# Optimization experiments

Measured on AMD Instinct MI355X. Metric: run time of the kernel, lower is better.

The kernel has to match this reference:

```python
import jax, jax.numpy as jnp
import numpy as np

B = 2048; SQ = 64; PC = 24; F = 16; H = 128; D = 256; T = 128; A = 4672
NSQ = B * SQ; NPC = B * PC


def setup_inputs() -> dict:
    key = jax.random.key(0)
    ks = iter(jax.random.split(key, 48))
    def nrm(shape, s=0.05):
        return jax.random.normal(next(ks), shape, dtype=jnp.float32) * s
    def edges(e_per, src_per, dst_per):
        # per-graph local edges: graph_offset + local node index
        g = jnp.repeat(jnp.arange(B), e_per)
        src = g * src_per + jax.random.randint(next(ks), (B * e_per,), 0, src_per)
        dst = g * dst_per + jax.random.randint(next(ks), (B * e_per,), 0, dst_per)
        return jnp.stack([src, dst]).astype(jnp.int32)
    gp = jnp.repeat(jnp.arange(B), PC)
    occ_src = jnp.arange(NPC, dtype=jnp.int32)                       # each piece occupies one square
    occ_dst = (gp * SQ + jax.random.randint(next(ks), (NPC,), 0, SQ)).astype(jnp.int32)
    ei_occ = jnp.stack([occ_src, occ_dst])                           # piece -> square
    ei_rev = ei_occ[::-1]                                            # square -> piece (rev_occupied_by)
    return dict(
        x_sq=jax.random.normal(next(ks), (NSQ, F), dtype=jnp.float32),
        x_pc=jax.random.normal(next(ks), (NPC, F), dtype=jnp.float32),
        W_in_sq=nrm((F, H)), b_in_sq=jnp.zeros((H,), jnp.float32),
        W_in_pc=nrm((F, H)), b_in_pc=jnp.zeros((H,), jnp.float32),
        W_adj=nrm((H, H)), W_occ=nrm((H, H)), W_att=nrm((H, H)), W_def=nrm((H, H)), W_rev=nrm((H, H)),
        W_out=nrm((H, D)), b_out=jnp.zeros((D,), jnp.float32),
        W_pt=nrm((D, T)), b_pt=jnp.zeros((T,), jnp.float32),
        W_vt=nrm((D, T)), b_vt=jnp.zeros((T,), jnp.float32),
        W_ph=nrm((T, A)), b_ph=jnp.zeros((A,), jnp.float32),
        W_vh=nrm((T, 1)), b_vh=jnp.zeros((1,), jnp.float32),
        ei_adj=edges(420, SQ, SQ),
        ei_occ=ei_occ,
        ei_att=edges(40, PC, PC),
        ei_def=edges(40, PC, PC),
        ei_rev=ei_rev,
        square_batch=jnp.repeat(jnp.arange(B), SQ).astype(jnp.int32),
        piece_batch=gp.astype(jnp.int32),
    )


def reference(x_sq, x_pc, W_in_sq, b_in_sq, W_in_pc, b_in_pc,
              W_adj, W_occ, W_att, W_def, W_rev, W_out, b_out,
              W_pt, b_pt, W_vt, b_vt, W_ph, b_ph, W_vh, b_vh,
              ei_adj, ei_occ, ei_att, ei_def, ei_rev, square_batch, piece_batch):
    gelu = jax.nn.gelu
    seg = jax.ops.segment_sum
    # per-node-type input encoders
    h_sq = gelu(x_sq @ W_in_sq + b_in_sq)          # [NSQ, H]
    h_pc = gelu(x_pc @ W_in_pc + b_in_pc)          # [NPC, H]
    # heterogeneous message passing: gather -> linear -> scatter-sum per edge type
    agg_sq = seg(h_sq[ei_adj[0]] @ W_adj, ei_adj[1], NSQ)
    agg_sq = agg_sq + seg(h_pc[ei_occ[0]] @ W_occ, ei_occ[1], NSQ)
    agg_pc = seg(h_pc[ei_att[0]] @ W_att, ei_att[1], NPC)
    agg_pc = agg_pc + seg(h_pc[ei_def[0]] @ W_def, ei_def[1], NPC)
    agg_pc = agg_pc + seg(h_sq[ei_rev[0]] @ W_rev, ei_rev[1], NPC)
    h_sq2 = gelu(h_sq + agg_sq)
    h_pc2 = gelu(h_pc + agg_pc)
    # project to embed_dim and mean-pool per graph
    out_sq = gelu(h_sq2 @ W_out + b_out)           # [NSQ, D]
    out_pc = gelu(h_pc2 @ W_out + b_out)           # [NPC, D]
    shared = seg(out_sq, square_batch, B) / SQ + seg(out_pc, piece_batch, B) / PC  # [B, D]
    # dual trunks + heads (exactly as in ChessNetwork.forward)
    policy_logits = gelu(shared @ W_pt + b_pt) @ W_ph + b_ph        # [B, 4672]
    value = jnp.tanh(gelu(shared @ W_vt + b_vt) @ W_vh + b_vh)      # [B, 1]
    return policy_logits, value
```

## Files before the change

### kernel.cpp

```cpp
#include <hip/hip_runtime.h>

#define BATCH 2048
#define SQN 64
#define PCN 24
#define FEAT 16
#define HID 128
#define DOUT 256
#define TDIM 128
#define ADIM 4672
#define NSQT (BATCH*SQN)
#define NPCT (BATCH*PCN)
#define E_ADJ 420
#define E_ATT 40
#define E_ADJ_TOT (BATCH*E_ADJ)
#define E_ATT_TOT (BATCH*E_ATT)

typedef unsigned short u16;
typedef unsigned int u32;
typedef __attribute__((ext_vector_type(8))) short bf16x8;
typedef __attribute__((ext_vector_type(8))) unsigned short u16x8;
typedef __attribute__((ext_vector_type(4))) float f32x4;
typedef __attribute__((ext_vector_type(2))) unsigned int u32x2;
typedef __attribute__((ext_vector_type(4))) unsigned int u32x4;

#define OFF_WADJ_H 0
#define OFF_WADJ_L 16384
#define OFF_WOCC_H 32768
#define OFF_WOCC_L 49152
#define OFF_WATT_H 65536
#define OFF_WATT_L 81920
#define OFF_WDEF_H 98304
#define OFF_WDEF_L 114688
#define OFF_WREV_H 131072
#define OFF_WREV_L 147456
#define OFF_WOUT_H 163840
#define OFF_WOUT_L 196608
#define OFF_WPH_H  229376
#define OFF_WPH_L  827392
#define OFF_WINSQ_H 1425408
#define OFF_WINSQ_L 1429504
#define OFF_WINPC_H 1433600
#define OFF_WINPC_L 1437696
#define WB_TOTAL    1441792

#define K_SMEM 81920

#define PHP_OFF  0
#define PAH_OFF  24576
#define PAL_OFF  36864
#define PEA_OFF  49152
#define PED_OFF  49472
#define PSA_OFF  49792
#define PSD_OFF  50112
#define PRSA_OFF 50432
#define PCUA_OFF 50692
#define PCNA_OFF 50948
#define PRSD_OFF 51204
#define PCUD_OFF 51464
#define PCND_OFF 51720
#define PRVS_OFF 51976
#define PRVD_OFF 52168

__device__ __forceinline__ u32 cvtpk(float a, float b) {
    u32 r;
    asm("v_cvt_pk_bf16_f32 %0, %1, %2" : "=v"(r) : "v"(a), "v"(b));
    return r;
}
__device__ __forceinline__ u16 f2b(float x) { return (u16)cvtpk(x, x); }
__device__ __forceinline__ float b2f(u16 h) { return __uint_as_float(((u32)h) << 16); }
__device__ __forceinline__ void split2(float x, u16& h, u16& l) {
    u32 wp = cvtpk(x, x);
    h = (u16)wp;
    float r = x - __uint_as_float(wp << 16);
    l = (u16)cvtpk(r, r);
}
__device__ __forceinline__ void split_pk(float a, float b, u32& wh, u32& wl) {
    wh = cvtpk(a, b);
    float ra = a - __uint_as_float(wh << 16);
    float rb = b - __uint_as_float(wh & 0xffff0000u);
    wl = cvtpk(ra, rb);
}
__device__ __forceinline__ float gelu_f(float x) {
    float x2 = x * x;
    float z2 = x * __builtin_fmaf(x2, 0.0713548162f, 1.5957691216f);
    float e = __expf(z2);
    return x - x * __fdividef(1.0f, e + 1.0f);
}
__device__ __forceinline__ f32x4 MFMA(bf16x8 a, bf16x8 b, f32x4 c) {
    return __builtin_amdgcn_mfma_f32_16x16x32_bf16(a, b, c, 0, 0, 0);
}
__device__ __forceinline__ bf16x8 bzero() {
    bf16x8 v = {0,0,0,0,0,0,0,0}; return v;
}
__device__ __forceinline__ void xfrag(const float* __restrict__ xrow, int g,
                                      bf16x8& ah, bf16x8& al)
{
    const f32x4 a = *(const f32x4*)(xrow + g*8);
    const f32x4 b = *(const f32x4*)(xrow + g*8 + 4);
    u32 h0,h1,h2,h3,l0,l1,l2,l3;
    split_pk(a[0], a[1], h0, l0);
    split_pk(a[2], a[3], h1, l1);
    split_pk(b[0], b[1], h2, l2);
    split_pk(b[2], b[3], h3, l3);
    u32x4 vh = {h0,h1,h2,h3};
    u32x4 vl = {l0,l1,l2,l3};
    ah = *(bf16x8*)&vh;
    al = *(bf16x8*)&vl;
}

template<int NT, int RT>
__device__ __forceinline__ void gemm_nt(
    const unsigned char* Ah, const unsigned char* Al,
    const u16* __restrict__ wh, const u16* __restrict__ wl,
    int ntBase, int lane, int g, int lr, f32x4 (&c)[NT][RT])
{
    const int sw = lr << 4;
    #pragma unroll
    for (int ks = 0; ks < 4; ++ks) {
        const int ko = ks*64 + g*16;
        bf16x8 ah[RT], al[RT];
        #pragma unroll
        for (int rt = 0; rt < RT; ++rt) {
            const int ro = (rt*16 + lr)*256 + (ko ^ sw);
            ah[rt] = *(const bf16x8*)(Ah + ro);
            al[rt] = *(const bf16x8*)(Al + ro);
        }
        #pragma unroll
        for (int ntl = 0; ntl < NT; ++ntl) {
            bf16x8 bh = *(const bf16x8*)(wh + (((ntBase+ntl)*4 + ks)*64 + lane)*8);
            bf16x8 bl = *(const bf16x8*)(wl + (((ntBase+ntl)*4 + ks)*64 + lane)*8);
            #pragma unroll
            for (int rt = 0; rt < RT; ++rt) {
                c[ntl][rt] = MFMA(ah[rt], bh, c[ntl][rt]);
                c[ntl][rt] = MFMA(al[rt], bh, c[ntl][rt]);
                c[ntl][rt] = MFMA(ah[rt], bl, c[ntl][rt]);
            }
        }
    }
}

__device__ __forceinline__ void gather_f32_8(
    const unsigned char* H, const int* srt, int st, int en, int cq8, float (&acc)[16])
{
    for (int i = st; i < en; ++i) {
        const int s = srt[i];
        const unsigned char* rp = H + s*512;
        const int sw2 = (s & 15) << 4;
        #pragma unroll
        for (int u = 0; u < 4; ++u) {
            f32x4 v = *(const f32x4*)(rp + ((cq8*64 + u*16) ^ sw2));
            acc[u*4+0] += v[0]; acc[u*4+1] += v[1];
            acc[u*4+2] += v[2]; acc[u*4+3] += v[3];
        }
    }
}
__device__ __forceinline__ void writeA_8(
    unsigned char* Ah, unsigned char* Al, int d, int cq8, const float (&acc)[16])
{
    unsigned char* wh = Ah + d*256;
    unsigned char* wl = Al + d*256;
    const int dw = (d & 15) << 4;
    #pragma unroll
    for (int u = 0; u < 2; ++u) {
        u32 oh[4], ol[4];
        #pragma unroll
        for (int j = 0; j < 4; ++j)
            split_pk(acc[u*8 + j*2], acc[u*8 + j*2 + 1], oh[j], ol[j]);
        u32x4 vh = {oh[0], oh[1], oh[2], oh[3]};
        u32x4 vl = {ol[0], ol[1], ol[2], ol[3]};
        *(u32x4*)(wh + ((cq8*32 + u*16) ^ dw)) = vh;
        *(u32x4*)(wl + ((cq8*32 + u*16) ^ dw)) = vl;
    }
}

__global__ __launch_bounds__(256) void k_prep(
    const float* __restrict__ W_adj, const float* __restrict__ W_occ,
    const float* __restrict__ W_att, const float* __restrict__ W_def,
    const float* __restrict__ W_rev, const float* __restrict__ W_out,
    const float* __restrict__ W_ph,
    const float* __restrict__ W_in_sq, const float* __restrict__ W_in_pc,
    u16* __restrict__ wb)
{
    int gid = blockIdx.x*256 + threadIdx.x;
    int fid = gid >> 6, lane = gid & 63;
    int g8 = (lane >> 4) * 8, lr = lane & 15;
    u16x8 vh, vl;
    if (fid >= 1392) {
        int f = fid - 1392;
        const float* src = (f < 8) ? W_in_sq : W_in_pc;
        int oh = (f < 8) ? OFF_WINSQ_H : OFF_WINPC_H;
        int ol = (f < 8) ? OFF_WINSQ_L : OFF_WINPC_L;
        int nt = f & 7;
        int col = nt*16 + lr;
        #pragma unroll
        for (int j = 0; j < 8; ++j) {
            int k = g8 + j;
            float v = (k < 16) ? src[k*HID + col] : 0.f;
            u16 h, l; split2(v, h, l);
            vh[j] = h; vl[j] = l;
        }
        *(u16x8*)(wb + oh + (nt*64 + lane)*8) = vh;
        *(u16x8*)(wb + ol + (nt*64 + lane)*8) = vl;
        return;
    }
    const float* src; int ld, f, oh, ol;
    if (fid < 32)       { src = W_adj; ld = HID;  f = fid;      oh = OFF_WADJ_H; ol = OFF_WADJ_L; }
    else if (fid < 64)  { src = W_occ; ld = HID;  f = fid-32;   oh = OFF_WOCC_H; ol = OFF_WOCC_L; }
    else if (fid < 96)  { src = W_att; ld = HID;  f = fid-64;   oh = OFF_WATT_H; ol = OFF_WATT_L; }
    else if (fid < 128) { src = W_def; ld = HID;  f = fid-96;   oh = OFF_WDEF_H; ol = OFF_WDEF_L; }
    else if (fid < 160) { src = W_rev; ld = HID;  f = fid-128;  oh = OFF_WREV_H; ol = OFF_WREV_L; }
    else if (fid < 224) { src = W_out; ld = DOUT; f = fid-160;  oh = OFF_WOUT_H; ol = OFF_WOUT_L; }
    else                { src = W_ph;  ld = ADIM; f = fid-224;  oh = OFF_WPH_H;  ol = OFF_WPH_L; }
    int nt = f >> 2, kb = f & 3;
    int col = nt*16 + lr;
    #pragma unroll
    for (int j = 0; j < 8; ++j) {
        int k = kb*32 + g8 + j;
        u16 h, l; split2(src[k*ld + col], h, l);
        vh[j] = h; vl[j] = l;
    }
    *(u16x8*)(wb + oh + (f*64 + lane)*8) = vh;
    *(u16x8*)(wb + ol + (f*64 + lane)*8) = vl;
}

__device__ __forceinline__ void sq_path(
    unsigned char* SMb, int b, int t,
    const float* __restrict__ x_sq, const float* __restrict__ x_pc,
    const float* __restrict__ b_in_sq, const float* __restrict__ b_in_pc,
    const float* __restrict__ b_out,
    const int* __restrict__ ei_adj, const int* __restrict__ ei_occ,
    const u16* __restrict__ wb, float* __restrict__ shared_sq)
{
    unsigned char* Hs_h  = SMb;
    unsigned char* Hs_l  = SMb + 16384;
    int*           Mint  = (int*)(SMb + 32768);
    unsigned char* HOT_h = SMb + 32768;
    unsigned char* HOT_l = SMb + 40960;
    unsigned char* Mocc  = SMb + 49152;
    unsigned char* A_h   = SMb + 32768;
    unsigned char* A_l   = SMb + 49152;
    unsigned char* Madj  = SMb + 65536;
    unsigned char* Hp    = SMb + 73728;

    const int w = t >> 6, lane = t & 63, g = lane >> 4, lr = lane & 15;
    const int colp = w*16 + lr;

    #pragma unroll
    for (int i = 0; i < 8; ++i) Mint[t + i*512] = 0;
    ((u32*)Mocc)[t] = 0;
    ((u32*)Mocc)[t + 512] = 0;
    ((u32*)(Hp + 6144))[t] = 0;
    __syncthreads();

    for (int i = t; i < E_ADJ; i += 512) {
        int s = ei_adj[b*E_ADJ + i] - b*SQN;
        int d = ei_adj[E_ADJ_TOT + b*E_ADJ + i] - b*SQN;
        atomicAdd(&Mint[d*64 + s], 1);
    }
    if (t < PCN) {
        int p = ei_occ[b*PCN + t] - b*PCN;
        int d = ei_occ[NPCT + b*PCN + t] - b*SQN;
        *(u16*)(Mocc + d*64 + ((p*2) ^ ((d&3)<<4))) = 0x3F80;
    }
    __syncthreads();

    #pragma unroll
    for (int ii = 0; ii < 4; ++ii) {
        int i = t + ii*512;
        int row = i >> 5, cp = i & 31;
        float v0 = (float)Mint[row*64 + cp*2];
        float v1 = (float)Mint[row*64 + cp*2 + 1];
        *(u32*)(Madj + row*128 + ((cp*4) ^ ((row&7)<<4))) = cvtpk(v0, v1);
    }
    float hv[16];
    {
        const f32x4 z = {0.f,0.f,0.f,0.f};
        f32x4 ch[4] = {z,z,z,z};
        {
            bf16x8 bh = *(const bf16x8*)(wb + OFF_WINSQ_H + (w*64 + lane)*8);
            bf16x8 bl = *(const bf16x8*)(wb + OFF_WINSQ_L + (w*64 + lane)*8);
            #pragma unroll
            for (int rt = 0; rt < 4; ++rt) {
                bf16x8 ah = bzero(), al = bzero();
                if (g < 2) xfrag(x_sq + (b*SQN + rt*16 + lr)*FEAT, g, ah, al);
                ch[rt] = MFMA(ah, bh, ch[rt]);
                ch[rt] = MFMA(al, bh, ch[rt]);
                ch[rt] = MFMA(ah, bl, ch[rt]);
            }
        }
        const float bbs = b_in_sq[colp];
        #pragma unroll
        for (int rt = 0; rt < 4; ++rt)
            #pragma unroll
            for (int r = 0; r < 4; ++r) {
                const int row = rt*16 + g*4 + r;
                float h = gelu_f(ch[rt][r] + bbs);
                hv[rt*4 + r] = h;
                u16 hh, ll; split2(h, hh, ll);
                const int bo = row*256 + ((colp*2) ^ ((row&15)<<4));
                *(u16*)(Hs_h + bo) = hh;
                *(u16*)(Hs_l + bo) = ll;
            }
        f32x4 cp2[2] = {z, z};
        {
            bf16x8 bh = *(const bf16x8*)(wb + OFF_WINPC_H + (w*64 + lane)*8);
            bf16x8 bl = *(const bf16x8*)(wb + OFF_WINPC_L + (w*64 + lane)*8);
            #pragma unroll
            for (int rt = 0; rt < 2; ++rt) {
                const int row = rt*16 + lr;
                bf16x8 ah = bzero(), al = bzero();
                if (g < 2 && row < PCN) xfrag(x_pc + (b*PCN + row)*FEAT, g, ah, al);
                cp2[rt] = MFMA(ah, bh, cp2[rt]);
                cp2[rt] = MFMA(al, bh, cp2[rt]);
                cp2[rt] = MFMA(ah, bl, cp2[rt]);
            }
        }
        const float bbp = b_in_pc[colp];
        #pragma unroll
        for (int rt = 0; rt < 2; ++rt)
            #pragma unroll
            for (int r = 0; r < 4; ++r) {
                const int row = rt*16 + g*4 + r;
                if (row < PCN) {
                    float h = gelu_f(cp2[rt][r] + bbp);
                    *(u16*)(Hp + row*256 + ((colp*2) ^ ((row&15)<<4))) = f2b(h);
                }
            }
    }
    __syncthreads();

    f32x4 hwj[4], hwo[2];
    {
        const f32x4 z = {0.f,0.f,0.f,0.f};
        hwj[0]=z; hwj[1]=z; hwj[2]=z; hwj[3]=z; hwo[0]=z; hwo[1]=z;
        const int sw15 = lr << 4;
        #pragma unroll
        for (int ks = 0; ks < 4; ++ks) {
            const int ko = ks*64 + g*16;
            bf16x8 bh = *(const bf16x8*)(wb + OFF_WADJ_H + ((w*4 + ks)*64 + lane)*8);
            bf16x8 bl = *(const bf16x8*)(wb + OFF_WADJ_L + ((w*4 + ks)*64 + lane)*8);
            #pragma unroll
            for (int rt = 0; rt < 4; ++rt) {
                const int ro = (rt*16 + lr)*256 + (ko ^ sw15);
                bf16x8 ah = *(const bf16x8*)(Hs_h + ro);
                bf16x8 al = *(const bf16x8*)(Hs_l + ro);
                hwj[rt] = MFMA(ah, bh, hwj[rt]);
                hwj[rt] = MFMA(al, bh, hwj[rt]);
                hwj[rt] = MFMA(ah, bl, hwj[rt]);
            }
            bf16x8 oh = *(const bf16x8*)(wb + OFF_WOCC_H + ((w*4 + ks)*64 + lane)*8);
            bf16x8 ol = *(const bf16x8*)(wb + OFF_WOCC_L + ((w*4 + ks)*64 + lane)*8);
            #pragma unroll
            for (int rt = 0; rt < 2; ++rt) {
                const int ro = (rt*16 + lr)*256 + (ko ^ sw15);
                bf16x8 ah = *(const bf16x8*)(Hp + ro);
                hwo[rt] = MFMA(ah, oh, hwo[rt]);
                hwo[rt] = MFMA(ah, ol, hwo[rt]);
            }
        }
    }
    __syncthreads();

    {
        const int swj = (lr & 7) << 4;
        #pragma unroll
        for (int rt = 0; rt < 4; ++rt) {
            u32 h01, l01, h23, l23;
            split_pk(hwj[rt][0], hwj[rt][1], h01, l01);
            split_pk(hwj[rt][2], hwj[rt][3], h23, l23);
            const int off = colp*128 + ((rt*32 + g*8) ^ swj);
            *(u32x2*)(Hs_h + off) = (u32x2){h01, h23};
            *(u32x2*)(Hs_l + off) = (u32x2){l01, l23};
        }
        const int swo = (lr & 3) << 4;
        #pragma unroll
        for (int rt = 0; rt < 2; ++rt) {
            u32 h01, l01, h23, l23;
            split_pk(hwo[rt][0], hwo[rt][1], h01, l01);
            split_pk(hwo[rt][2], hwo[rt][3], h23, l23);
            const int off = colp*64 + ((rt*32 + g*8) ^ swo);
            *(u32x2*)(HOT_h + off) = (u32x2){h01, h23};
            *(u32x2*)(HOT_l + off) = (u32x2){l01, l23};
        }
    }
    __syncthreads();

    f32x4 c1[4];
    {
        const f32x4 z = {0.f,0.f,0.f,0.f};
        c1[0]=z; c1[1]=z; c1[2]=z; c1[3]=z;
        const int swj = (lr & 7) << 4;
        #pragma unroll
        for (int ks = 0; ks < 2; ++ks) {
            const int bo = colp*128 + ((ks*64 + g*16) ^ swj);
            bf16x8 bh = *(const bf16x8*)(Hs_h + bo);
            bf16x8 bl = *(const bf16x8*)(Hs_l + bo);
            #pragma unroll
            for (int rt = 0; rt < 4; ++rt) {
                const int ao = (rt*16 + lr)*128 + ((ks*64 + g*16) ^ swj);
                bf16x8 am = *(const bf16x8*)(Madj + ao);
                c1[rt] = MFMA(am, bh, c1[rt]);
                c1[rt] = MFMA(am, bl, c1[rt]);
            }
        }
        const int swo = (lr & 3) << 4;
        {
            const int bo = colp*64 + ((g*16) ^ swo);
            bf16x8 bh = *(const bf16x8*)(HOT_h + bo);
            bf16x8 bl = *(const bf16x8*)(HOT_l + bo);
            #pragma unroll
            for (int rt = 0; rt < 4; ++rt) {
                const int ao = (rt*16 + lr)*64 + ((g*16) ^ swo);
                bf16x8 am = *(const bf16x8*)(Mocc + ao);
                c1[rt] = MFMA(am, bh, c1[rt]);
                c1[rt] = MFMA(am, bl, c1[rt]);
            }
        }
    }
    __syncthreads();

    #pragma unroll
    for (int rt = 0; rt < 4; ++rt)
        #pragma unroll
        for (int r = 0; r < 4; ++r) {
            const int row = rt*16 + g*4 + r;
            float h2 = gelu_f(c1[rt][r] + hv[rt*4 + r]);
            u16 hh, ll; split2(h2, hh, ll);
            const int bo = row*256 + ((colp*2) ^ ((row&15)<<4));
            *(u16*)(A_h + bo) = hh;
            *(u16*)(A_l + bo) = ll;
        }
    __syncthreads();

    f32x4 c2[2][4];
    {
        const f32x4 z = {0.f,0.f,0.f,0.f};
        #pragma unroll
        for (int n = 0; n < 2; ++n)
            #pragma unroll
            for (int rt = 0; rt < 4; ++rt) c2[n][rt] = z;
    }
    gemm_nt<2,4>(A_h, A_l, wb + OFF_WOUT_H, wb + OFF_WOUT_L, w*2, lane, g, lr, c2);
    #pragma unroll
    for (int ntl = 0; ntl < 2; ++ntl) {
        const int col = (w*2 + ntl)*16 + lr;
        const float bias = b_out[col];
        float cs = 0.f;
        #pragma unroll
        for (int rt = 0; rt < 4; ++rt)
            #pragma unroll
            for (int r = 0; r < 4; ++r) cs += gelu_f(c2[ntl][rt][r] + bias);
        cs += __shfl_xor(cs, 16);
        cs += __shfl_xor(cs, 32);
        if (lane < 16) shared_sq[b*DOUT + col] = cs * (1.0f/64.0f);
    }
}

__device__ __forceinline__ void pc_path(
    unsigned char* SMb, int pcb, int t,
    const float* __restrict__ x_sq, const float* __restrict__ x_pc,
    const float* __restrict__ b_in_sq, const float* __restrict__ b_in_pc,
    const float* __restrict__ b_out,
    const int* __restrict__ ei_att, const int* __restrict__ ei_def,
    const int* __restrict__ ei_rev,
    const u16* __restrict__ wb, float* __restrict__ shared_pc)
{
    unsigned char* Hp = SMb + PHP_OFF;
    unsigned char* Ah = SMb + PAH_OFF;
    unsigned char* Al = SMb + PAL_OFF;
    int* ea_pk = (int*)(SMb + PEA_OFF);
    int* ed_pk = (int*)(SMb + PED_OFF);
    int* srt_a = (int*)(SMb + PSA_OFF);
    int* srt_d = (int*)(SMb + PSD_OFF);
    int* rs_a  = (int*)(SMb + PRSA_OFF);
    int* cur_a = (int*)(SMb + PCUA_OFF);
    int* cnt_a = (int*)(SMb + PCNA_OFF);
    int* rs_d  = (int*)(SMb + PRSD_OFF);
    int* cur_d = (int*)(SMb + PCUD_OFF);
    int* cnt_d = (int*)(SMb + PCND_OFF);
    int* rv_s  = (int*)(SMb + PRVS_OFF);
    int* rv_d  = (int*)(SMb + PRVD_OFF);

    const int w = t >> 6, lane = t & 63, g = lane >> 4, lr = lane & 15;
    const int NR = 2*PCN;

    for (int i = t; i < 2*E_ATT; i += 512) {
        int sb = (i >= E_ATT) ? 1 : 0;
        int e = i - sb*E_ATT;
        int gb = pcb*2 + sb;
        int ro = sb*PCN - gb*PCN;
        int s = ei_att[gb*E_ATT + e] + ro;
        int d = ei_att[E_ATT_TOT + gb*E_ATT + e] + ro;
        ea_pk[i] = s | (d << 16);
        s = ei_def[gb*E_ATT + e] + ro;
        d = ei_def[E_ATT_TOT + gb*E_ATT + e] + ro;
        ed_pk[i] = s | (d << 16);
    }
    if (t < NR) {
        int sb = (t >= PCN) ? 1 : 0;
        int gb = pcb*2 + sb;
        int p = t - sb*PCN;
        rv_s[t] = ei_rev[gb*PCN + p];
        rv_d[t] = ei_rev[NPCT + gb*PCN + p] - gb*PCN + sb*PCN;
    }
    if (t < 64) { cnt_a[t] = 0; cnt_d[t] = 0; }
    __syncthreads();

    for (int i = t; i < 2*E_ATT; i += 512) {
        atomicAdd(&cnt_a[ea_pk[i] >> 16], 1);
        atomicAdd(&cnt_d[ed_pk[i] >> 16], 1);
    }
    __syncthreads();

    if (t < 64) {
        int v = cnt_a[t], o0 = v;
        for (int o = 1; o < 64; o <<= 1) { int u = __shfl_up(v, o); if (t >= o) v += u; }
        rs_a[t+1] = v; cur_a[t] = v - o0; if (t == 0) rs_a[0] = 0;
    } else if (t < 128) {
        int l = t - 64;
        int v = cnt_d[l], o0 = v;
        for (int o = 1; o < 64; o <<= 1) { int u = __shfl_up(v, o); if (l >= o) v += u; }
        rs_d[l+1] = v; cur_d[l] = v - o0; if (l == 0) rs_d[0] = 0;
    }
    __syncthreads();

    for (int i = t; i < 2*E_ATT; i += 512) {
        int pk = ea_pk[i];
        int p = atomicAdd(&cur_a[pk >> 16], 1); srt_a[p] = pk & 0xffff;
        pk = ed_pk[i];
        p = atomicAdd(&cur_d[pk >> 16], 1); srt_d[p] = pk & 0xffff;
    }
    {
        const int colp = w*16 + lr;
        const f32x4 z = {0.f,0.f,0.f,0.f};
        f32x4 cp[3] = {z,z,z};
        {
            bf16x8 bh = *(const bf16x8*)(wb + OFF_WINPC_H + (w*64 + lane)*8);
            bf16x8 bl = *(const bf16x8*)(wb + OFF_WINPC_L + (w*64 + lane)*8);
            #pragma unroll
            for (int rt = 0; rt < 3; ++rt) {
                bf16x8 ah = bzero(), al = bzero();
                if (g < 2) xfrag(x_pc + (pcb*NR + rt*16 + lr)*FEAT, g, ah, al);
                cp[rt] = MFMA(ah, bh, cp[rt]);
                cp[rt] = MFMA(al, bh, cp[rt]);
                cp[rt] = MFMA(ah, bl, cp[rt]);
            }
        }
        const float bbp = b_in_pc[colp];
        #pragma unroll
        for (int rt = 0; rt < 3; ++rt)
            #pragma unroll
            for (int r = 0; r < 4; ++r) {
                const int row = rt*16 + g*4 + r;
                float h = gelu_f(cp[rt][r] + bbp);
                *(float*)(Hp + row*512 + ((colp*4) ^ ((row&15)<<4))) = h;
            }
        f32x4 cr[3] = {z,z,z};
        {
            bf16x8 bh = *(const bf16x8*)(wb + OFF_WINSQ_H + (w*64 + lane)*8);
            bf16x8 bl = *(const bf16x8*)(wb + OFF_WINSQ_L + (w*64 + lane)*8);
            #pragma unroll
            for (int rt = 0; rt < 3; ++rt) {
                bf16x8 ah = bzero(), al = bzero();
                if (g < 2) {
                    int gr = rv_s[rt*16 + lr];
                    xfrag(x_sq + gr*FEAT, g, ah, al);
                }
                cr[rt] = MFMA(ah, bh, cr[rt]);
                cr[rt] = MFMA(al, bh, cr[rt]);
                cr[rt] = MFMA(ah, bl, cr[rt]);
            }
        }
        const float bbs = b_in_sq[colp];
        #pragma unroll
        for (int rt = 0; rt < 3; ++rt)
            #pragma unroll
            for (int r = 0; r < 4; ++r) {
                const int row0 = rt*16 + g*4 + r;
                const int dr = rv_d[row0];
                float h = gelu_f(cr[rt][r] + bbs);
                u16 hh, ll; split2(h, hh, ll);
                const int bo = dr*256 + ((colp*2) ^ ((dr&15)<<4));
                *(u16*)(Ah + bo) = hh;
                *(u16*)(Al + bo) = ll;
            }
    }
    __syncthreads();

    f32x4 c1[1][3];
    {
        const f32x4 z = {0.f,0.f,0.f,0.f};
        #pragma unroll
        for (int rt = 0; rt < 3; ++rt) c1[0][rt] = z;
    }
    gemm_nt<1,3>(Ah, Al, wb + OFF_WREV_H, wb + OFF_WREV_L, w, lane, g, lr, c1);
    __syncthreads();

    {
        const int d = t >> 3, cq8 = t & 7;
        if (d < NR) {
            float acc[16];
            #pragma unroll
            for (int i = 0; i < 16; ++i) acc[i] = 0.f;
            gather_f32_8(Hp, srt_a, rs_a[d], rs_a[d+1], cq8, acc);
            writeA_8(Ah, Al, d, cq8, acc);
        }
    }
    __syncthreads();

    gemm_nt<1,3>(Ah, Al, wb + OFF_WATT_H, wb + OFF_WATT_L, w, lane, g, lr, c1);
    __syncthreads();

    {
        const int d = t >> 3, cq8 = t & 7;
        if (d < NR) {
            float acc[16];
            #pragma unroll
            for (int i = 0; i < 16; ++i) acc[i] = 0.f;
            gather_f32_8(Hp, srt_d, rs_d[d], rs_d[d+1], cq8, acc);
            writeA_8(Ah, Al, d, cq8, acc);
        }
    }
    __syncthreads();

    gemm_nt<1,3>(Ah, Al, wb + OFF_WDEF_H, wb + OFF_WDEF_L, w, lane, g, lr, c1);
    __syncthreads();

    {
        const int colp = w*16 + lr;
        #pragma unroll
        for (int rt = 0; rt < 3; ++rt)
            #pragma unroll
            for (int r = 0; r < 4; ++r) {
                const int row = rt*16 + g*4 + r;
                float hvv = *(const float*)(Hp + row*512 + ((colp*4) ^ ((row&15)<<4)));
                float h2 = gelu_f(c1[0][rt][r] + hvv);
                u16 hh, ll; split2(h2, hh, ll);
                const int bo = row*256 + ((colp*2) ^ ((row&15)<<4));
                *(u16*)(Ah + bo) = hh;
                *(u16*)(Al + bo) = ll;
            }
    }
    __syncthreads();

    f32x4 c2[2][3];
    {
        const f32x4 z = {0.f,0.f,0.f,0.f};
        #pragma unroll
        for (int n = 0; n < 2; ++n)
            #pragma unroll
            for (int rt = 0; rt < 3; ++rt) c2[n][rt] = z;
    }
    gemm_nt<2,3>(Ah, Al, wb + OFF_WOUT_H, wb + OFF_WOUT_L, w*2, lane, g, lr, c2);
    #pragma unroll
    for (int ntl = 0; ntl < 2; ++ntl) {
        const int col = (w*2 + ntl)*16 + lr;
        const float bias = b_out[col];
        float s0 = 0.f, s1 = 0.f;
        #pragma unroll
        for (int r = 0; r < 4; ++r) s0 += gelu_f(c2[ntl][0][r] + bias);
        {
            float tt = 0.f;
            #pragma unroll
            for (int r = 0; r < 4; ++r) tt += gelu_f(c2[ntl][1][r] + bias);
            s0 += (g < 2) ? tt : 0.f;
            s1 += (g < 2) ? 0.f : tt;
        }
        #pragma unroll
        for (int r = 0; r < 4; ++r) s1 += gelu_f(c2[ntl][2][r] + bias);
        s0 += __shfl_xor(s0, 16); s0 += __shfl_xor(s0, 32);
        s1 += __shfl_xor(s1, 16); s1 += __shfl_xor(s1, 32);
        if (lane < 16) {
            const int b0 = pcb*2, b1 = b0 + 1;
            shared_pc[b0*DOUT + col] = s0 * (1.0f/PCN);
            shared_pc[b1*DOUT + col] = s1 * (1.0f/PCN);
        }
    }
}

__global__ __launch_bounds__(512, 4) void k_main(
    const float* __restrict__ x_sq, const float* __restrict__ x_pc,
    const float* __restrict__ b_in_sq, const float* __restrict__ b_in_pc,
    const float* __restrict__ b_out,
    const int* __restrict__ ei_adj, const int* __restrict__ ei_occ,
    const int* __restrict__ ei_att, const int* __restrict__ ei_def,
    const int* __restrict__ ei_rev,
    const u16* __restrict__ wb,
    float* __restrict__ shared_sq, float* __restrict__ shared_pc)
{
    extern __shared__ __align__(16) unsigned char SMb[];
    const int bid = blockIdx.x;
    const int grp = bid / 3, rem = bid - grp*3;
    if (rem < 2) {
        sq_path(SMb, grp*2 + rem, threadIdx.x, x_sq, x_pc, b_in_sq, b_in_pc,
                b_out, ei_adj, ei_occ, wb, shared_sq);
    } else {
        pc_path(SMb, grp, threadIdx.x, x_sq, x_pc, b_in_sq, b_in_pc,
                b_out, ei_att, ei_def, ei_rev, wb, shared_pc);
    }
}

__global__ __launch_bounds__(256) void k_head(
    const float* __restrict__ shared_sq, const float* __restrict__ shared_pc,
    const float* __restrict__ W_pt, const float* __restrict__ b_pt,
    const float* __restrict__ W_vt, const float* __restrict__ b_vt,
    const float* __restrict__ W_vh, const float* __restrict__ b_vh,
    u16* __restrict__ tpol_h, u16* __restrict__ tpol_l, float* __restrict__ out_value)
{
    __shared__ float sh[2*DOUT];
    __shared__ float vred[2*TDIM];
    const int t = threadIdx.x;
    const int hh = t >> 7, j = t & 127;
    const int b = blockIdx.x*2 + hh;
    for (int i = t; i < 2*DOUT; i += 256)
        sh[i] = shared_sq[blockIdx.x*2*DOUT + i] + shared_pc[blockIdx.x*2*DOUT + i];
    __syncthreads();
    const float* s = sh + hh*DOUT;
    float ap = b_pt[j], av = b_vt[j];
    #pragma unroll 8
    for (int k = 0; k < DOUT; ++k) {
        float sv = s[k];
        ap += sv * W_pt[k*TDIM + j];
        av += sv * W_vt[k*TDIM + j];
    }
    float tv = gelu_f(ap);
    u16 th, tl; split2(tv, th, tl);
    tpol_h[b*TDIM + j] = th;
    tpol_l[b*TDIM + j] = tl;
    vred[hh*TDIM + j] = gelu_f(av) * W_vh[j];
    __syncthreads();
    for (int stp = 64; stp > 0; stp >>= 1) {
        if (j < stp) vred[hh*TDIM + j] += vred[hh*TDIM + j + stp];
        __syncthreads();
    }
    if (j == 0) out_value[b] = tanhf(vred[hh*TDIM] + b_vh[0]);
}

__global__ __launch_bounds__(256) void k_pol(
    const u16* __restrict__ tpol_h, const u16* __restrict__ tpol_l,
    const u16* __restrict__ wb, const float* __restrict__ b_ph,
    float* __restrict__ pol)
{
    const u16* wph_h = wb + OFF_WPH_H;
    const u16* wph_l = wb + OFF_WPH_L;
    const int t = threadIdx.x, w = t >> 6, lane = t & 63, g = lane >> 4, lr = lane & 15;
    const int nt = blockIdx.x*4 + w;
    const int rbase = blockIdx.y*64;
    f32x4 acc[4];
    const f32x4 z = {0.f,0.f,0.f,0.f};
    #pragma unroll
    for (int rt = 0; rt < 4; ++rt) acc[rt] = z;
    #pragma unroll
    for (int ks = 0; ks < 4; ++ks) {
        bf16x8 bh = *(const bf16x8*)(wph_h + ((nt*4 + ks)*64 + lane)*8);
        bf16x8 bl = *(const bf16x8*)(wph_l + ((nt*4 + ks)*64 + lane)*8);
        #pragma unroll
        for (int rt = 0; rt < 4; ++rt) {
            const int ro = (rbase + rt*16 + lr)*TDIM + ks*32 + g*8;
            bf16x8 ah = *(const bf16x8*)(tpol_h + ro);
            bf16x8 al = *(const bf16x8*)(tpol_l + ro);
            acc[rt] = MFMA(ah, bh, acc[rt]);
            acc[rt] = MFMA(al, bh, acc[rt]);
            acc[rt] = MFMA(ah, bl, acc[rt]);
        }
    }
    const float bias = b_ph[nt*16 + lr];
    #pragma unroll
    for (int rt = 0; rt < 4; ++rt)
        #pragma unroll
        for (int r = 0; r < 4; ++r) {
            int row = rbase + rt*16 + g*4 + r;
            pol[(size_t)row*ADIM + nt*16 + lr] = acc[rt][r] + bias;
        }
}

extern "C" void kernel_launch(void* const* d_in, const int* in_sizes, int n_in,
                              void* d_out, int out_size, void* d_ws, size_t ws_size,
                              hipStream_t stream) {
    (void)in_sizes; (void)n_in; (void)out_size; (void)ws_size;
    const float* x_sq    = (const float*)d_in[0];
    const float* x_pc    = (const float*)d_in[1];
    const float* W_in_sq = (const float*)d_in[2];
    const float* b_in_sq = (const float*)d_in[3];
    const float* W_in_pc = (const float*)d_in[4];
    const float* b_in_pc = (const float*)d_in[5];
    const float* W_adj   = (const float*)d_in[6];
    const float* W_occ   = (const float*)d_in[7];
    const float* W_att   = (const float*)d_in[8];
    const float* W_def   = (const float*)d_in[9];
    const float* W_rev   = (const float*)d_in[10];
    const float* W_out   = (const float*)d_in[11];
    const float* b_out   = (const float*)d_in[12];
    const float* W_pt    = (const float*)d_in[13];
    const float* b_pt    = (const float*)d_in[14];
    const float* W_vt    = (const float*)d_in[15];
    const float* b_vt    = (const float*)d_in[16];
    const float* W_ph    = (const float*)d_in[17];
    const float* b_ph    = (const float*)d_in[18];
    const float* W_vh    = (const float*)d_in[19];
    const float* b_vh    = (const float*)d_in[20];
    const int* ei_adj    = (const int*)d_in[21];
    const int* ei_occ    = (const int*)d_in[22];
    const int* ei_att    = (const int*)d_in[23];
    const int* ei_def    = (const int*)d_in[24];
    const int* ei_rev    = (const int*)d_in[25];

    float* out = (float*)d_out;
    float* pol = out;
    float* val = out + (size_t)BATCH * ADIM;

    float* shared_sq = (float*)d_ws;
    float* shared_pc = shared_sq + BATCH*DOUT;
    u16* tpol_h = (u16*)(shared_pc + BATCH*DOUT);
    u16* tpol_l = tpol_h + BATCH*TDIM;
    u16* wb     = tpol_l + BATCH*TDIM;

    hipFuncSetAttribute((const void*)k_main,
                        hipFuncAttributeMaxDynamicSharedMemorySize, K_SMEM);

    k_prep<<<352, 256, 0, stream>>>(W_adj, W_occ, W_att, W_def, W_rev, W_out, W_ph,
                                    W_in_sq, W_in_pc, wb);
    k_main<<<3072, 512, K_SMEM, stream>>>(x_sq, x_pc, b_in_sq, b_in_pc, b_out,
                                          ei_adj, ei_occ, ei_att, ei_def, ei_rev,
                                          wb, shared_sq, shared_pc);
    k_head<<<BATCH/2, 256, 0, stream>>>(shared_sq, shared_pc, W_pt, b_pt, W_vt, b_vt,
                                        W_vh, b_vh, tpol_h, tpol_l, val);
    k_pol<<<dim3(ADIM/64, BATCH/64), 256, 0, stream>>>(tpol_h, tpol_l, wb, b_ph, pol);
}
```

Before: 198.2 us.

## Double k_main threads per block and move trunk GEMMs to MFMA

k_main now launches 1024 threads per block instead of 512. Wave work is re-split so each wave covers half the row tiles of one column tile, and the pc path's shared-memory layout is enlarged. Separately, the policy and value trunk projections in k_head become split-bf16 MFMA GEMMs over 32-row tiles, with weights pre-packed in k_prep, replacing the scalar per-thread dot products. The aim is more waves in flight per block and tensor-core use in the head, at the cost of more A-fragment reloads from LDS and possible occupancy limits at 1024 threads with 80KB LDS.

```diff
diff --git a/kernel.cpp b/kernel.cpp
--- a/kernel.cpp
+++ b/kernel.cpp
@@ -41,25 +41,29 @@
 #define OFF_WINSQ_L 1429504
 #define OFF_WINPC_H 1433600
 #define OFF_WINPC_L 1437696
-#define WB_TOTAL    1441792
+#define OFF_WPT_H  1441792
+#define OFF_WPT_L  1474560
+#define OFF_WVT_H  1507328
+#define OFF_WVT_L  1540096
+#define WB_TOTAL   1572864
 
 #define K_SMEM 81920
 
 #define PHP_OFF  0
-#define PAH_OFF  24576
-#define PAL_OFF  36864
-#define PEA_OFF  49152
-#define PED_OFF  49472
-#define PSA_OFF  49792
-#define PSD_OFF  50112
-#define PRSA_OFF 50432
-#define PCUA_OFF 50692
-#define PCNA_OFF 50948
-#define PRSD_OFF 51204
-#define PCUD_OFF 51464
-#define PCND_OFF 51720
-#define PRVS_OFF 51976
-#define PRVD_OFF 52168
+#define PAH_OFF  32768
+#define PAL_OFF  49152
+#define PEA_OFF  65536
+#define PED_OFF  65856
+#define PSA_OFF  66176
+#define PSD_OFF  66496
+#define PRSA_OFF 66816
+#define PCUA_OFF 67076
+#define PCNA_OFF 67332
+#define PRSD_OFF 67588
+#define PCUD_OFF 67848
+#define PCND_OFF 68104
+#define PRVS_OFF 68360
+#define PRVD_OFF 68616
 
 __device__ __forceinline__ u32 cvtpk(float a, float b) {
     u32 r;
@@ -112,65 +116,55 @@
 __device__ __forceinline__ void gemm_nt(
     const unsigned char* Ah, const unsigned char* Al,
     const u16* __restrict__ wh, const u16* __restrict__ wl,
-    int ntBase, int lane, int g, int lr, f32x4 (&c)[NT][RT])
+    int ntBase, int rowBase, int lane, int g, int lr, f32x4 (&c)[NT][RT])
 {
     const int sw = lr << 4;
     #pragma unroll
     for (int ks = 0; ks < 4; ++ks) {
-        const int ko = ks*64 + g*16;
-        bf16x8 ah[RT], al[RT];
-        #pragma unroll
-        for (int rt = 0; rt < RT; ++rt) {
-            const int ro = (rt*16 + lr)*256 + (ko ^ sw);
-            ah[rt] = *(const bf16x8*)(Ah + ro);
-            al[rt] = *(const bf16x8*)(Al + ro);
-        }
+        const int ko = (ks*64 + g*16) ^ sw;
         #pragma unroll
         for (int ntl = 0; ntl < NT; ++ntl) {
             bf16x8 bh = *(const bf16x8*)(wh + (((ntBase+ntl)*4 + ks)*64 + lane)*8);
             bf16x8 bl = *(const bf16x8*)(wl + (((ntBase+ntl)*4 + ks)*64 + lane)*8);
             #pragma unroll
             for (int rt = 0; rt < RT; ++rt) {
-                c[ntl][rt] = MFMA(ah[rt], bh, c[ntl][rt]);
-                c[ntl][rt] = MFMA(al[rt], bh, c[ntl][rt]);
-                c[ntl][rt] = MFMA(ah[rt], bl, c[ntl][rt]);
-            }
-        }
-    }
-}
-
-__device__ __forceinline__ void gather_f32_8(
-    const unsigned char* H, const int* srt, int st, int en, int cq8, float (&acc)[16])
+                const int ro = ((rowBase+rt)*16 + lr)*256 + ko;
+                bf16x8 ah = *(const bf16x8*)(Ah + ro);
+                bf16x8 al = *(const bf16x8*)(Al + ro);
+                c[ntl][rt] = MFMA(ah, bh, c[ntl][rt]);
+                c[ntl][rt] = MFMA(al, bh, c[ntl][rt]);
+                c[ntl][rt] = MFMA(ah, bl, c[ntl][rt]);
+            }
+        }
+    }
+}
+
+__device__ __forceinline__ void gather_f32_16(
+    const unsigned char* H, const int* srt, int st, int en, int cq, float (&acc)[8])
 {
     for (int i = st; i < en; ++i) {
         const int s = srt[i];
         const unsigned char* rp = H + s*512;
         const int sw2 = (s & 15) << 4;
         #pragma unroll
-        for (int u = 0; u < 4; ++u) {
-            f32x4 v = *(const f32x4*)(rp + ((cq8*64 + u*16) ^ sw2));
+        for (int u = 0; u < 2; ++u) {
+            f32x4 v = *(const f32x4*)(rp + ((cq*32 + u*16) ^ sw2));
             acc[u*4+0] += v[0]; acc[u*4+1] += v[1];
             acc[u*4+2] += v[2]; acc[u*4+3] += v[3];
         }
     }
 }
-__device__ __forceinline__ void writeA_8(
-    unsigned char* Ah, unsigned char* Al, int d, int cq8, const float (&acc)[16])
-{
-    unsigned char* wh = Ah + d*256;
-    unsigned char* wl = Al + d*256;
+__device__ __forceinline__ void writeA_16(
+    unsigned char* Ah, unsigned char* Al, int d, int cq, const float (&acc)[8])
+{
     const int dw = (d & 15) << 4;
-    #pragma unroll
-    for (int u = 0; u < 2; ++u) {
-        u32 oh[4], ol[4];
-        #pragma unroll
-        for (int j = 0; j < 4; ++j)
-            split_pk(acc[u*8 + j*2], acc[u*8 + j*2 + 1], oh[j], ol[j]);
-        u32x4 vh = {oh[0], oh[1], oh[2], oh[3]};
-        u32x4 vl = {ol[0], ol[1], ol[2], ol[3]};
-        *(u32x4*)(wh + ((cq8*32 + u*16) ^ dw)) = vh;
-        *(u32x4*)(wl + ((cq8*32 + u*16) ^ dw)) = vl;
-    }
+    u32 oh[4], ol[4];
+    #pragma unroll
+    for (int j = 0; j < 4; ++j) split_pk(acc[j*2], acc[j*2+1], oh[j], ol[j]);
+    u32x4 vh = {oh[0],oh[1],oh[2],oh[3]};
+    u32x4 vl = {ol[0],ol[1],ol[2],ol[3]};
+    *(u32x4*)(Ah + d*256 + ((cq*16) ^ dw)) = vh;
+    *(u32x4*)(Al + d*256 + ((cq*16) ^ dw)) = vl;
 }
 
 __global__ __launch_bounds__(256) void k_prep(
@@ -179,12 +173,31 @@
     const float* __restrict__ W_rev, const float* __restrict__ W_out,
     const float* __restrict__ W_ph,
     const float* __restrict__ W_in_sq, const float* __restrict__ W_in_pc,
+    const float* __restrict__ W_pt, const float* __restrict__ W_vt,
     u16* __restrict__ wb)
 {
     int gid = blockIdx.x*256 + threadIdx.x;
     int fid = gid >> 6, lane = gid & 63;
     int g8 = (lane >> 4) * 8, lr = lane & 15;
     u16x8 vh, vl;
+    if (fid >= 1408) {
+        int f = fid - 1408;
+        int which = f >> 6, f2 = f & 63;
+        const float* src = which ? W_vt : W_pt;
+        int oh = which ? OFF_WVT_H : OFF_WPT_H;
+        int ol = which ? OFF_WVT_L : OFF_WPT_L;
+        int nt = f2 >> 3, kb = f2 & 7;
+        int col = nt*16 + lr;
+        #pragma unroll
+        for (int j = 0; j < 8; ++j) {
+            int k = kb*32 + g8 + j;
+            u16 h, l; split2(src[k*TDIM + col], h, l);
+            vh[j] = h; vl[j] = l;
+        }
+        *(u16x8*)(wb + oh + (f2*64 + lane)*8) = vh;
+        *(u16x8*)(wb + ol + (f2*64 + lane)*8) = vl;
+        return;
+    }
     if (fid >= 1392) {
         int f = fid - 1392;
         const float* src = (f < 8) ? W_in_sq : W_in_pc;
@@ -243,16 +256,16 @@
     unsigned char* Hp    = SMb + 73728;
 
     const int w = t >> 6, lane = t & 63, g = lane >> 4, lr = lane & 15;
-    const int colp = w*16 + lr;
-
-    #pragma unroll
-    for (int i = 0; i < 8; ++i) Mint[t + i*512] = 0;
+    const int n2 = w >> 1, rh = w & 1, rtb = rh*2;
+    const int colp = n2*16 + lr;
+
+    #pragma unroll
+    for (int ii = 0; ii < 4; ++ii) Mint[t + ii*1024] = 0;
     ((u32*)Mocc)[t] = 0;
-    ((u32*)Mocc)[t + 512] = 0;
-    ((u32*)(Hp + 6144))[t] = 0;
-    __syncthreads();
-
-    for (int i = t; i < E_ADJ; i += 512) {
+    if (t < 512) ((u32*)(Hp + 6144))[t] = 0;
+    __syncthreads();
+
+    for (int i = t; i < E_ADJ; i += 1024) {
         int s = ei_adj[b*E_ADJ + i] - b*SQN;
         int d = ei_adj[E_ADJ_TOT + b*E_ADJ + i] - b*SQN;
         atomicAdd(&Mint[d*64 + s], 1);
@@ -265,24 +278,24 @@
     __syncthreads();
 
     #pragma unroll
-    for (int ii = 0; ii < 4; ++ii) {
-        int i = t + ii*512;
+    for (int ii = 0; ii < 2; ++ii) {
+        int i = t + ii*1024;
         int row = i >> 5, cp = i & 31;
         float v0 = (float)Mint[row*64 + cp*2];
         float v1 = (float)Mint[row*64 + cp*2 + 1];
         *(u32*)(Madj + row*128 + ((cp*4) ^ ((row&7)<<4))) = cvtpk(v0, v1);
     }
-    float hv[16];
+    float hv[8];
     {
         const f32x4 z = {0.f,0.f,0.f,0.f};
-        f32x4 ch[4] = {z,z,z,z};
+        f32x4 ch[2] = {z,z};
         {
-            bf16x8 bh = *(const bf16x8*)(wb + OFF_WINSQ_H + (w*64 + lane)*8);
-            bf16x8 bl = *(const bf16x8*)(wb + OFF_WINSQ_L + (w*64 + lane)*8);
-            #pragma unroll
-            for (int rt = 0; rt < 4; ++rt) {
+            bf16x8 bh = *(const bf16x8*)(wb + OFF_WINSQ_H + (n2*64 + lane)*8);
+            bf16x8 bl = *(const bf16x8*)(wb + OFF_WINSQ_L + (n2*64 + lane)*8);
+            #pragma unroll
+            for (int rt = 0; rt < 2; ++rt) {
                 bf16x8 ah = bzero(), al = bzero();
-                if (g < 2) xfrag(x_sq + (b*SQN + rt*16 + lr)*FEAT, g, ah, al);
+                if (g < 2) xfrag(x_sq + (b*SQN + (rtb+rt)*16 + lr)*FEAT, g, ah, al);
                 ch[rt] = MFMA(ah, bh, ch[rt]);
                 ch[rt] = MFMA(al, bh, ch[rt]);
                 ch[rt] = MFMA(ah, bl, ch[rt]);
@@ -290,10 +303,10 @@
         }
         const float bbs = b_in_sq[colp];
         #pragma unroll
-        for (int rt = 0; rt < 4; ++rt)
+        for (int rt = 0; rt < 2; ++rt)
             #pragma unroll
             for (int r = 0; r < 4; ++r) {
-                const int row = rt*16 + g*4 + r;
+                const int row = (rtb+rt)*16 + g*4 + r;
                 float h = gelu_f(ch[rt][r] + bbs);
                 hv[rt*4 + r] = h;
                 u16 hh, ll; split2(h, hh, ll);
@@ -301,61 +314,55 @@
                 *(u16*)(Hs_h + bo) = hh;
                 *(u16*)(Hs_l + bo) = ll;
             }
-        f32x4 cp2[2] = {z, z};
+        f32x4 cp2 = z;
         {
-            bf16x8 bh = *(const bf16x8*)(wb + OFF_WINPC_H + (w*64 + lane)*8);
-            bf16x8 bl = *(const bf16x8*)(wb + OFF_WINPC_L + (w*64 + lane)*8);
+            bf16x8 bh = *(const bf16x8*)(wb + OFF_WINPC_H + (n2*64 + lane)*8);
+            bf16x8 bl = *(const bf16x8*)(wb + OFF_WINPC_L + (n2*64 + lane)*8);
+            const int row0 = rh*16 + lr;
+            bf16x8 ah = bzero(), al = bzero();
+            if (g < 2 && row0 < PCN) xfrag(x_pc + (b*PCN + row0)*FEAT, g, ah, al);
+            cp2 = MFMA(ah, bh, cp2);
+            cp2 = MFMA(al, bh, cp2);
+            cp2 = MFMA(ah, bl, cp2);
+        }
+        const float bbp = b_in_pc[colp];
+        #pragma unroll
+        for (int r = 0; r < 4; ++r) {
+            const int row = rh*16 + g*4 + r;
+            if (row < PCN) {
+                float h = gelu_f(cp2[r] + bbp);
+                *(u16*)(Hp + row*256 + ((colp*2) ^ ((row&15)<<4))) = f2b(h);
+            }
+        }
+    }
+    __syncthreads();
+
+    f32x4 hwj[2], hwo;
+    {
+        const f32x4 z = {0.f,0.f,0.f,0.f};
+        hwj[0]=z; hwj[1]=z; hwo=z;
+        const int sw15 = lr << 4;
+        #pragma unroll
+        for (int ks = 0; ks < 4; ++ks) {
+            const int ko = (ks*64 + g*16) ^ sw15;
+            bf16x8 bh = *(const bf16x8*)(wb + OFF_WADJ_H + ((n2*4 + ks)*64 + lane)*8);
+            bf16x8 bl = *(const bf16x8*)(wb + OFF_WADJ_L + ((n2*4 + ks)*64 + lane)*8);
             #pragma unroll
             for (int rt = 0; rt < 2; ++rt) {
-                const int row = rt*16 + lr;
-                bf16x8 ah = bzero(), al = bzero();
-                if (g < 2 && row < PCN) xfrag(x_pc + (b*PCN + row)*FEAT, g, ah, al);
-                cp2[rt] = MFMA(ah, bh, cp2[rt]);
-                cp2[rt] = MFMA(al, bh, cp2[rt]);
-                cp2[rt] = MFMA(ah, bl, cp2[rt]);
-            }
-        }
-        const float bbp = b_in_pc[colp];
-        #pragma unroll
-        for (int rt = 0; rt < 2; ++rt)
-            #pragma unroll
-            for (int r = 0; r < 4; ++r) {
-                const int row = rt*16 + g*4 + r;
-                if (row < PCN) {
-                    float h = gelu_f(cp2[rt][r] + bbp);
-                    *(u16*)(Hp + row*256 + ((colp*2) ^ ((row&15)<<4))) = f2b(h);
-                }
-            }
-    }
-    __syncthreads();
-
-    f32x4 hwj[4], hwo[2];
-    {
-        const f32x4 z = {0.f,0.f,0.f,0.f};
-        hwj[0]=z; hwj[1]=z; hwj[2]=z; hwj[3]=z; hwo[0]=z; hwo[1]=z;
-        const int sw15 = lr << 4;
-        #pragma unroll
-        for (int ks = 0; ks < 4; ++ks) {
-            const int ko = ks*64 + g*16;
-            bf16x8 bh = *(const bf16x8*)(wb + OFF_WADJ_H + ((w*4 + ks)*64 + lane)*8);
-            bf16x8 bl = *(const bf16x8*)(wb + OFF_WADJ_L + ((w*4 + ks)*64 + lane)*8);
-            #pragma unroll
-            for (int rt = 0; rt < 4; ++rt) {
-                const int ro = (rt*16 + lr)*256 + (ko ^ sw15);
+                const int ro = ((rtb+rt)*16 + lr)*256 + ko;
                 bf16x8 ah = *(const bf16x8*)(Hs_h + ro);
                 bf16x8 al = *(const bf16x8*)(Hs_l + ro);
                 hwj[rt] = MFMA(ah, bh, hwj[rt]);
                 hwj[rt] = MFMA(al, bh, hwj[rt]);
                 hwj[rt] = MFMA(ah, bl, hwj[rt]);
             }
-            bf16x8 oh = *(const bf16x8*)(wb + OFF_WOCC_H + ((w*4 + ks)*64 + lane)*8);
-            bf16x8 ol = *(const bf16x8*)(wb + OFF_WOCC_L + ((w*4 + ks)*64 + lane)*8);
-            #pragma unroll
-            for (int rt = 0; rt < 2; ++rt) {
-                const int ro = (rt*16 + lr)*256 + (ko ^ sw15);
+            bf16x8 oh = *(const bf16x8*)(wb + OFF_WOCC_H + ((n2*4 + ks)*64 + lane)*8);
+            bf16x8 ol = *(const bf16x8*)(wb + OFF_WOCC_L + ((n2*4 + ks)*64 + lane)*8);
+            {
+                const int ro = (rh*16 + lr)*256 + ko;
                 bf16x8 ah = *(const bf16x8*)(Hp + ro);
-                hwo[rt] = MFMA(ah, oh, hwo[rt]);
-                hwo[rt] = MFMA(ah, ol, hwo[rt]);
+                hwo = MFMA(ah, oh, hwo);
+                hwo = MFMA(ah, ol, hwo);
             }
         }
     }
@@ -364,31 +371,30 @@
     {
         const int swj = (lr & 7) << 4;
         #pragma unroll
-        for (int rt = 0; rt < 4; ++rt) {
+        for (int rt = 0; rt < 2; ++rt) {
             u32 h01, l01, h23, l23;
             split_pk(hwj[rt][0], hwj[rt][1], h01, l01);
             split_pk(hwj[rt][2], hwj[rt][3], h23, l23);
-            const int off = colp*128 + ((rt*32 + g*8) ^ swj);
+            const int off = colp*128 + (((rtb+rt)*32 + g*8) ^ swj);
             *(u32x2*)(Hs_h + off) = (u32x2){h01, h23};
             *(u32x2*)(Hs_l + off) = (u32x2){l01, l23};
         }
         const int swo = (lr & 3) << 4;
-        #pragma unroll
-        for (int rt = 0; rt < 2; ++rt) {
+        {
             u32 h01, l01, h23, l23;
-            split_pk(hwo[rt][0], hwo[rt][1], h01, l01);
-            split_pk(hwo[rt][2], hwo[rt][3], h23, l23);
-            const int off = colp*64 + ((rt*32 + g*8) ^ swo);
+            split_pk(hwo[0], hwo[1], h01, l01);
+            split_pk(hwo[2], hwo[3], h23, l23);
+            const int off = colp*64 + ((rh*32 + g*8) ^ swo);
             *(u32x2*)(HOT_h + off) = (u32x2){h01, h23};
             *(u32x2*)(HOT_l + off) = (u32x2){l01, l23};
         }
     }
     __syncthreads();
 
-    f32x4 c1[4];
+    f32x4 c1[2];
     {
         const f32x4 z = {0.f,0.f,0.f,0.f};
-        c1[0]=z; c1[1]=z; c1[2]=z; c1[3]=z;
+        c1[0]=z; c1[1]=z;
         const int swj = (lr & 7) << 4;
         #pragma unroll
         for (int ks = 0; ks < 2; ++ks) {
@@ -396,8 +402,8 @@
             bf16x8 bh = *(const bf16x8*)(Hs_h + bo);
             bf16x8 bl = *(const bf16x8*)(Hs_l + bo);
             #pragma unroll
-            for (int rt = 0; rt < 4; ++rt) {
-                const int ao = (rt*16 + lr)*128 + ((ks*64 + g*16) ^ swj);
+            for (int rt = 0; rt < 2; ++rt) {
+                const int ao = ((rtb+rt)*16 + lr)*128 + ((ks*64 + g*16) ^ swj);
                 bf16x8 am = *(const bf16x8*)(Madj + ao);
                 c1[rt] = MFMA(am, bh, c1[rt]);
                 c1[rt] = MFMA(am, bl, c1[rt]);
@@ -409,8 +415,8 @@
             bf16x8 bh = *(const bf16x8*)(HOT_h + bo);
             bf16x8 bl = *(const bf16x8*)(HOT_l + bo);
             #pragma unroll
-            for (int rt = 0; rt < 4; ++rt) {
-                const int ao = (rt*16 + lr)*64 + ((g*16) ^ swo);
+            for (int rt = 0; rt < 2; ++rt) {
+                const int ao = ((rtb+rt)*16 + lr)*64 + ((g*16) ^ swo);
                 bf16x8 am = *(const bf16x8*)(Mocc + ao);
                 c1[rt] = MFMA(am, bh, c1[rt]);
                 c1[rt] = MFMA(am, bl, c1[rt]);
@@ -420,10 +426,10 @@
     __syncthreads();
 
     #pragma unroll
-    for (int rt = 0; rt < 4; ++rt)
+    for (int rt = 0; rt < 2; ++rt)
         #pragma unroll
         for (int r = 0; r < 4; ++r) {
-            const int row = rt*16 + g*4 + r;
+            const int row = (rtb+rt)*16 + g*4 + r;
             float h2 = gelu_f(c1[rt][r] + hv[rt*4 + r]);
             u16 hh, ll; split2(h2, hh, ll);
             const int bo = row*256 + ((colp*2) ^ ((row&15)<<4));
@@ -432,24 +438,21 @@
         }
     __syncthreads();
 
-    f32x4 c2[2][4];
+    f32x4 c2[1][4];
     {
         const f32x4 z = {0.f,0.f,0.f,0.f};
         #pragma unroll
-        for (int n = 0; n < 2; ++n)
-            #pragma unroll
-            for (int rt = 0; rt < 4; ++rt) c2[n][rt] = z;
-    }
-    gemm_nt<2,4>(A_h, A_l, wb + OFF_WOUT_H, wb + OFF_WOUT_L, w*2, lane, g, lr, c2);
-    #pragma unroll
-    for (int ntl = 0; ntl < 2; ++ntl) {
-        const int col = (w*2 + ntl)*16 + lr;
+        for (int rt = 0; rt < 4; ++rt) c2[0][rt] = z;
+    }
+    gemm_nt<1,4>(A_h, A_l, wb + OFF_WOUT_H, wb + OFF_WOUT_L, w, 0, lane, g, lr, c2);
+    {
+        const int col = w*16 + lr;
         const float bias = b_out[col];
         float cs = 0.f;
         #pragma unroll
         for (int rt = 0; rt < 4; ++rt)
             #pragma unroll
-            for (int r = 0; r < 4; ++r) cs += gelu_f(c2[ntl][rt][r] + bias);
+            for (int r = 0; r < 4; ++r) cs += gelu_f(c2[0][rt][r] + bias);
         cs += __shfl_xor(cs, 16);
         cs += __shfl_xor(cs, 32);
         if (lane < 16) shared_sq[b*DOUT + col] = cs * (1.0f/64.0f);
@@ -482,13 +485,14 @@
     int* rv_d  = (int*)(SMb + PRVD_OFF);
 
     const int w = t >> 6, lane = t & 63, g = lane >> 4, lr = lane & 15;
-    const int NR = 2*PCN;
-
-    for (int i = t; i < 2*E_ATT; i += 512) {
+    const int n2 = w >> 1, rh = w & 1, rtb = rh*2;
+    const int colp = n2*16 + lr;
+
+    for (int i = t; i < 2*E_ATT; i += 1024) {
         int sb = (i >= E_ATT) ? 1 : 0;
         int e = i - sb*E_ATT;
         int gb = pcb*2 + sb;
-        int ro = sb*PCN - gb*PCN;
+        int ro = 32*sb - gb*PCN;
         int s = ei_att[gb*E_ATT + e] + ro;
         int d = ei_att[E_ATT_TOT + gb*E_ATT + e] + ro;
         ea_pk[i] = s | (d << 16);
@@ -496,17 +500,17 @@
         d = ei_def[E_ATT_TOT + gb*E_ATT + e] + ro;
         ed_pk[i] = s | (d << 16);
     }
-    if (t < NR) {
-        int sb = (t >= PCN) ? 1 : 0;
-        int gb = pcb*2 + sb;
-        int p = t - sb*PCN;
-        rv_s[t] = ei_rev[gb*PCN + p];
-        rv_d[t] = ei_rev[NPCT + gb*PCN + p] - gb*PCN + sb*PCN;
-    }
-    if (t < 64) { cnt_a[t] = 0; cnt_d[t] = 0; }
-    __syncthreads();
-
-    for (int i = t; i < 2*E_ATT; i += 512) {
+    if (t < 64) {
+        int sb = t >> 5, pr = t & 31, gb = pcb*2 + sb;
+        if (pr < PCN) {
+            rv_s[t] = ei_rev[gb*PCN + pr];
+            rv_d[t] = ei_rev[NPCT + gb*PCN + pr] - gb*PCN + 32*sb;
+        } else { rv_s[t] = 0; rv_d[t] = 0; }
+        cnt_a[t] = 0; cnt_d[t] = 0;
+    }
+    __syncthreads();
+
+    for (int i = t; i < 2*E_ATT; i += 1024) {
         atomicAdd(&cnt_a[ea_pk[i] >> 16], 1);
         atomicAdd(&cnt_d[ed_pk[i] >> 16], 1);
     }
@@ -524,23 +528,25 @@
     }
     __syncthreads();
 
-    for (int i = t; i < 2*E_ATT; i += 512) {
+    for (int i = t; i < 2*E_ATT; i += 1024) {
         int pk = ea_pk[i];
         int p = atomicAdd(&cur_a[pk >> 16], 1); srt_a[p] = pk & 0xffff;
         pk = ed_pk[i];
         p = atomicAdd(&cur_d[pk >> 16], 1); srt_d[p] = pk & 0xffff;
     }
-    {
-        const int colp = w*16 + lr;
+    float hv[8];
+    {
         const f32x4 z = {0.f,0.f,0.f,0.f};
-        f32x4 cp[3] = {z,z,z};
+        f32x4 cp[2] = {z,z};
         {
-            bf16x8 bh = *(const bf16x8*)(wb + OFF_WINPC_H + (w*64 + lane)*8);
-            bf16x8 bl = *(const bf16x8*)(wb + OFF_WINPC_L + (w*64 + lane)*8);
-            #pragma unroll
-            for (int rt = 0; rt < 3; ++rt) {
+            bf16x8 bh = *(const bf16x8*)(wb + OFF_WINPC_H + (n2*64 + lane)*8);
+            bf16x8 bl = *(const bf16x8*)(wb + OFF_WINPC_L + (n2*64 + lane)*8);
+            #pragma unroll
+            for (int rt = 0; rt < 2; ++rt) {
+                const int pr = rt*16 + lr;
                 bf16x8 ah = bzero(), al = bzero();
-                if (g < 2) xfrag(x_pc + (pcb*NR + rt*16 + lr)*FEAT, g, ah, al);
+                if (g < 2 && pr < PCN)
+                    xfrag(x_pc + ((pcb*2 + rh)*PCN + pr)*FEAT, g, ah, al);
                 cp[rt] = MFMA(ah, bh, cp[rt]);
                 cp[rt] = MFMA(al, bh, cp[rt]);
                 cp[rt] = MFMA(ah, bl, cp[rt]);
@@ -548,22 +554,27 @@
         }
         const float bbp = b_in_pc[colp];
         #pragma unroll
-        for (int rt = 0; rt < 3; ++rt)
+        for (int rt = 0; rt < 2; ++rt)
             #pragma unroll
             for (int r = 0; r < 4; ++r) {
-                const int row = rt*16 + g*4 + r;
+                const int pr = rt*16 + g*4 + r;
                 float h = gelu_f(cp[rt][r] + bbp);
-                *(float*)(Hp + row*512 + ((colp*4) ^ ((row&15)<<4))) = h;
-            }
-        f32x4 cr[3] = {z,z,z};
+                hv[rt*4 + r] = h;
+                if (pr < PCN) {
+                    const int row = rh*32 + pr;
+                    *(float*)(Hp + row*512 + ((colp*4) ^ ((row&15)<<4))) = h;
+                }
+            }
+        f32x4 cr[2] = {z,z};
         {
-            bf16x8 bh = *(const bf16x8*)(wb + OFF_WINSQ_H + (w*64 + lane)*8);
-            bf16x8 bl = *(const bf16x8*)(wb + OFF_WINSQ_L + (w*64 + lane)*8);
-            #pragma unroll
-            for (int rt = 0; rt < 3; ++rt) {
+            bf16x8 bh = *(const bf16x8*)(wb + OFF_WINSQ_H + (n2*64 + lane)*8);
+            bf16x8 bl = *(const bf16x8*)(wb + OFF_WINSQ_L + (n2*64 + lane)*8);
+            #pragma unroll
+            for (int rt = 0; rt < 2; ++rt) {
+                const int pr = rt*16 + lr;
                 bf16x8 ah = bzero(), al = bzero();
-                if (g < 2) {
-                    int gr = rv_s[rt*16 + lr];
+                if (g < 2 && pr < PCN) {
+                    int gr = rv_s[rh*32 + pr];
                     xfrag(x_sq + gr*FEAT, g, ah, al);
                 }
                 cr[rt] = MFMA(ah, bh, cr[rt]);
@@ -573,112 +584,95 @@
         }
         const float bbs = b_in_sq[colp];
         #pragma unroll
-        for (int rt = 0; rt < 3; ++rt)
+        for (int rt = 0; rt < 2; ++rt)
             #pragma unroll
             for (int r = 0; r < 4; ++r) {
-                const int row0 = rt*16 + g*4 + r;
-                const int dr = rv_d[row0];
-                float h = gelu_f(cr[rt][r] + bbs);
-                u16 hh, ll; split2(h, hh, ll);
-                const int bo = dr*256 + ((colp*2) ^ ((dr&15)<<4));
-                *(u16*)(Ah + bo) = hh;
-                *(u16*)(Al + bo) = ll;
-            }
-    }
-    __syncthreads();
-
-    f32x4 c1[1][3];
+                const int pr = rt*16 + g*4 + r;
+                if (pr < PCN) {
+                    const int dr = rv_d[rh*32 + pr];
+                    float h = gelu_f(cr[rt][r] + bbs);
+                    u16 hh, ll; split2(h, hh, ll);
+                    const int bo = dr*256 + ((colp*2) ^ ((dr&15)<<4));
+                    *(u16*)(Ah + bo) = hh;
+                    *(u16*)(Al + bo) = ll;
+                }
+            }
+    }
+    __syncthreads();
+
+    f32x4 c1[1][2];
     {
         const f32x4 z = {0.f,0.f,0.f,0.f};
-        #pragma unroll
-        for (int rt = 0; rt < 3; ++rt) c1[0][rt] = z;
-    }
-    gemm_nt<1,3>(Ah, Al, wb + OFF_WREV_H, wb + OFF_WREV_L, w, lane, g, lr, c1);
-    __syncthreads();
-
-    {
-        const int d = t >> 3, cq8 = t & 7;
-        if (d < NR) {
-            float acc[16];
-            #pragma unroll
-            for (int i = 0; i < 16; ++i) acc[i] = 0.f;
-            gather_f32_8(Hp, srt_a, rs_a[d], rs_a[d+1], cq8, acc);
-            writeA_8(Ah, Al, d, cq8, acc);
-        }
-    }
-    __syncthreads();
-
-    gemm_nt<1,3>(Ah, Al, wb + OFF_WATT_H, wb + OFF_WATT_L, w, lane, g, lr, c1);
-    __syncthreads();
-
-    {
-        const int d = t >> 3, cq8 = t & 7;
-        if (d < NR) {
-            float acc[16];
-            #pragma unroll
-            for (int i = 0; i < 16; ++i) acc[i] = 0.f;
-            gather_f32_8(Hp, srt_d, rs_d[d], rs_d[d+1], cq8, acc);
-            writeA_8(Ah, Al, d, cq8, acc);
-        }
-    }
-    __syncthreads();
-
-    gemm_nt<1,3>(Ah, Al, wb + OFF_WDEF_H, wb + OFF_WDEF_L, w, lane, g, lr, c1);
-    __syncthreads();
-
-    {
-        const int colp = w*16 + lr;
-        #pragma unroll
-        for (int rt = 0; rt < 3; ++rt)
-            #pragma unroll
-            for (int r = 0; r < 4; ++r) {
-                const int row = rt*16 + g*4 + r;
-                float hvv = *(const float*)(Hp + row*512 + ((colp*4) ^ ((row&15)<<4)));
-                float h2 = gelu_f(c1[0][rt][r] + hvv);
-                u16 hh, ll; split2(h2, hh, ll);
-                const int bo = row*256 + ((colp*2) ^ ((row&15)<<4));
-                *(u16*)(Ah + bo) = hh;
-                *(u16*)(Al + bo) = ll;
-            }
-    }
-    __syncthreads();
-
-    f32x4 c2[2][3];
+        c1[0][0] = z; c1[0][1] = z;
+    }
+    gemm_nt<1,2>(Ah, Al, wb + OFF_WREV_H, wb + OFF_WREV_L, n2, rtb, lane, g, lr, c1);
+    __syncthreads();
+
+    {
+        const int d = t >> 4, cq = t & 15;
+        float acc[8];
+        #pragma unroll
+        for (int i = 0; i < 8; ++i) acc[i] = 0.f;
+        gather_f32_16(Hp, srt_a, rs_a[d], rs_a[d+1], cq, acc);
+        writeA_16(Ah, Al, d, cq, acc);
+    }
+    __syncthreads();
+
+    gemm_nt<1,2>(Ah, Al, wb + OFF_WATT_H, wb + OFF_WATT_L, n2, rtb, lane, g, lr, c1);
+    __syncthreads();
+
+    {
+        const int d = t >> 4, cq = t & 15;
+        float acc[8];
+        #pragma unroll
+        for (int i = 0; i < 8; ++i) acc[i] = 0.f;
+        gather_f32_16(Hp, srt_d, rs_d[d], rs_d[d+1], cq, acc);
+        writeA_16(Ah, Al, d, cq, acc);
+    }
+    __syncthreads();
+
+    gemm_nt<1,2>(Ah, Al, wb + OFF_WDEF_H, wb + OFF_WDEF_L, n2, rtb, lane, g, lr, c1);
+    __syncthreads();
+
+    #pragma unroll
+    for (int rt = 0; rt < 2; ++rt)
+        #pragma unroll
+        for (int r = 0; r < 4; ++r) {
+            const int row = rh*32 + rt*16 + g*4 + r;
+            float h2 = gelu_f(c1[0][rt][r] + hv[rt*4 + r]);
+            u16 hh, ll; split2(h2, hh, ll);
+            const int bo = row*256 + ((colp*2) ^ ((row&15)<<4));
+            *(u16*)(Ah + bo) = hh;
+            *(u16*)(Al + bo) = ll;
+        }
+    __syncthreads();
+
+    f32x4 c2[2][2];
     {
         const f32x4 z = {0.f,0.f,0.f,0.f};
-        #pragma unroll
-        for (int n = 0; n < 2; ++n)
-            #pragma unroll
-            for (int rt = 0; rt < 3; ++rt) c2[n][rt] = z;
-    }
-    gemm_nt<2,3>(Ah, Al, wb + OFF_WOUT_H, wb + OFF_WOUT_L, w*2, lane, g, lr, c2);
+        c2[0][0]=z; c2[0][1]=z; c2[1][0]=z; c2[1][1]=z;
+    }
+    gemm_nt<2,2>(Ah, Al, wb + OFF_WOUT_H, wb + OFF_WOUT_L, n2*2, rtb, lane, g, lr, c2);
     #pragma unroll
     for (int ntl = 0; ntl < 2; ++ntl) {
-        const int col = (w*2 + ntl)*16 + lr;
+        const int col = (n2*2 + ntl)*16 + lr;
         const float bias = b_out[col];
-        float s0 = 0.f, s1 = 0.f;
-        #pragma unroll
-        for (int r = 0; r < 4; ++r) s0 += gelu_f(c2[ntl][0][r] + bias);
+        float cs = 0.f;
+        #pragma unroll
+        for (int r = 0; r < 4; ++r) cs += gelu_f(c2[ntl][0][r] + bias);
         {
             float tt = 0.f;
             #pragma unroll
             for (int r = 0; r < 4; ++r) tt += gelu_f(c2[ntl][1][r] + bias);
-            s0 += (g < 2) ? tt : 0.f;
-            s1 += (g < 2) ? 0.f : tt;
-        }
-        #pragma unroll
-        for (int r = 0; r < 4; ++r) s1 += gelu_f(c2[ntl][2][r] + bias);
-        s0 += __shfl_xor(s0, 16); s0 += __shfl_xor(s0, 32);
-        s1 += __shfl_xor(s1, 16); s1 += __shfl_xor(s1, 32);
-        if (lane < 16) {
-            const int b0 = pcb*2, b1 = b0 + 1;
-            shared_pc[b0*DOUT + col] = s0 * (1.0f/PCN);
-            shared_pc[b1*DOUT + col] = s1 * (1.0f/PCN);
-        }
-    }
-}
-
-__global__ __launch_bounds__(512, 4) void k_main(
+            cs += (g < 2) ? tt : 0.f;
+        }
+        cs += __shfl_xor(cs, 16);
+        cs += __shfl_xor(cs, 32);
+        if (lane < 16) shared_pc[(pcb*2 + rh)*DOUT + col] = cs * (1.0f/PCN);
+    }
+}
+
+__global__ __launch_bounds__(1024, 8) void k_main(
     const float* __restrict__ x_sq, const float* __restrict__ x_pc,
     const float* __restrict__ b_in_sq, const float* __restrict__ b_in_pc,
     const float* __restrict__ b_out,
@@ -700,40 +694,100 @@
     }
 }
 
-__global__ __launch_bounds__(256) void k_head(
+__global__ __launch_bounds__(512) void k_head(
     const float* __restrict__ shared_sq, const float* __restrict__ shared_pc,
-    const float* __restrict__ W_pt, const float* __restrict__ b_pt,
-    const float* __restrict__ W_vt, const float* __restrict__ b_vt,
+    const u16* __restrict__ wb,
+    const float* __restrict__ b_pt, const float* __restrict__ b_vt,
     const float* __restrict__ W_vh, const float* __restrict__ b_vh,
     u16* __restrict__ tpol_h, u16* __restrict__ tpol_l, float* __restrict__ out_value)
 {
-    __shared__ float sh[2*DOUT];
-    __shared__ float vred[2*TDIM];
+    __shared__ __align__(16) unsigned char SH[33792];
+    unsigned char* Ah = SH;
+    unsigned char* Al = SH + 16384;
+    float* vpart = (float*)(SH + 32768);
+
     const int t = threadIdx.x;
-    const int hh = t >> 7, j = t & 127;
-    const int b = blockIdx.x*2 + hh;
-    for (int i = t; i < 2*DOUT; i += 256)
-        sh[i] = shared_sq[blockIdx.x*2*DOUT + i] + shared_pc[blockIdx.x*2*DOUT + i];
-    __syncthreads();
-    const float* s = sh + hh*DOUT;
-    float ap = b_pt[j], av = b_vt[j];
-    #pragma unroll 8
-    for (int k = 0; k < DOUT; ++k) {
-        float sv = s[k];
-        ap += sv * W_pt[k*TDIM + j];
-        av += sv * W_vt[k*TDIM + j];
-    }
-    float tv = gelu_f(ap);
-    u16 th, tl; split2(tv, th, tl);
-    tpol_h[b*TDIM + j] = th;
-    tpol_l[b*TDIM + j] = tl;
-    vred[hh*TDIM + j] = gelu_f(av) * W_vh[j];
-    __syncthreads();
-    for (int stp = 64; stp > 0; stp >>= 1) {
-        if (j < stp) vred[hh*TDIM + j] += vred[hh*TDIM + j + stp];
-        __syncthreads();
-    }
-    if (j == 0) out_value[b] = tanhf(vred[hh*TDIM] + b_vh[0]);
+    const int w = t >> 6, lane = t & 63, g = lane >> 4, lr = lane & 15;
+    const int rbase = blockIdx.x * 32;
+
+    {
+        const int row = t >> 4, c0 = (t & 15) * 16;
+        const float* s1 = shared_sq + (size_t)(rbase + row)*DOUT + c0;
+        const float* s2 = shared_pc + (size_t)(rbase + row)*DOUT + c0;
+        const int sw = (row & 15) << 4;
+        #pragma unroll
+        for (int cc = 0; cc < 2; ++cc) {
+            f32x4 a = *(const f32x4*)(s1 + cc*8);
+            f32x4 b = *(const f32x4*)(s2 + cc*8);
+            f32x4 a2 = *(const f32x4*)(s1 + cc*8 + 4);
+            f32x4 b2 = *(const f32x4*)(s2 + cc*8 + 4);
+            float v0=a[0]+b[0], v1=a[1]+b[1], v2=a[2]+b[2], v3=a[3]+b[3];
+            float v4=a2[0]+b2[0], v5=a2[1]+b2[1], v6=a2[2]+b2[2], v7=a2[3]+b2[3];
+            u32 h0,h1,h2,h3,l0,l1,l2,l3;
+            split_pk(v0,v1,h0,l0); split_pk(v2,v3,h1,l1);
+            split_pk(v4,v5,h2,l2); split_pk(v6,v7,h3,l3);
+            u32x4 vh = {h0,h1,h2,h3};
+            u32x4 vl = {l0,l1,l2,l3};
+            *(u32x4*)(Ah + row*512 + ((c0*2 + cc*16) ^ sw)) = vh;
+            *(u32x4*)(Al + row*512 + ((c0*2 + cc*16) ^ sw)) = vl;
+        }
+    }
+    __syncthreads();
+
+    f32x4 cpt[2], cvt[2];
+    {
+        const f32x4 z = {0.f,0.f,0.f,0.f};
+        cpt[0]=z; cpt[1]=z; cvt[0]=z; cvt[1]=z;
+        const int sw = lr << 4;
+        #pragma unroll
+        for (int ks = 0; ks < 8; ++ks) {
+            const int ko = (ks*64 + g*16) ^ sw;
+            bf16x8 ph_ = *(const bf16x8*)(wb + OFF_WPT_H + ((w*8 + ks)*64 + lane)*8);
+            bf16x8 pl_ = *(const bf16x8*)(wb + OFF_WPT_L + ((w*8 + ks)*64 + lane)*8);
+            bf16x8 vh_ = *(const bf16x8*)(wb + OFF_WVT_H + ((w*8 + ks)*64 + lane)*8);
+            bf16x8 vl_ = *(const bf16x8*)(wb + OFF_WVT_L + ((w*8 + ks)*64 + lane)*8);
+            #pragma unroll
+            for (int rt = 0; rt < 2; ++rt) {
+                const int ao = (rt*16 + lr)*512 + ko;
+                bf16x8 ah = *(const bf16x8*)(Ah + ao);
+                bf16x8 al = *(const bf16x8*)(Al + ao);
+                cpt[rt] = MFMA(ah, ph_, cpt[rt]);
+                cpt[rt] = MFMA(al, ph_, cpt[rt]);
+                cpt[rt] = MFMA(ah, pl_, cpt[rt]);
+                cvt[rt] = MFMA(ah, vh_, cvt[rt]);
+                cvt[rt] = MFMA(al, vh_, cvt[rt]);
+                cvt[rt] = MFMA(ah, vl_, cvt[rt]);
+            }
+        }
+    }
+
+    {
+        const int col = w*16 + lr;
+        const float bpt = b_pt[col], bvt = b_vt[col], wvh = W_vh[col];
+        #pragma unroll
+        for (int rt = 0; rt < 2; ++rt)
+            #pragma unroll
+            for (int r = 0; r < 4; ++r) {
+                const int row = rt*16 + g*4 + r;
+                float tv = gelu_f(cpt[rt][r] + bpt);
+                u16 th, tl; split2(tv, th, tl);
+                tpol_h[(size_t)(rbase + row)*TDIM + col] = th;
+                tpol_l[(size_t)(rbase + row)*TDIM + col] = tl;
+                float vv = gelu_f(cvt[rt][r] + bvt) * wvh;
+                vv += __shfl_xor(vv, 1);
+                vv += __shfl_xor(vv, 2);
+                vv += __shfl_xor(vv, 4);
+                vv += __shfl_xor(vv, 8);
+                if (lr == 0) vpart[row*8 + w] = vv;
+            }
+    }
+    __syncthreads();
+    if (t < 32) {
+        float s = 0.f;
+        #pragma unroll
+        for (int j = 0; j < 8; ++j) s += vpart[t*8 + j];
+        out_value[rbase + t] = tanhf(s + b_vh[0]);
+    }
 }
 
 __global__ __launch_bounds__(256) void k_pol(
@@ -818,12 +872,12 @@
     hipFuncSetAttribute((const void*)k_main,
                         hipFuncAttributeMaxDynamicSharedMemorySize, K_SMEM);
 
-    k_prep<<<352, 256, 0, stream>>>(W_adj, W_occ, W_att, W_def, W_rev, W_out, W_ph,
-                                    W_in_sq, W_in_pc, wb);
-    k_main<<<3072, 512, K_SMEM, stream>>>(x_sq, x_pc, b_in_sq, b_in_pc, b_out,
-                                          ei_adj, ei_occ, ei_att, ei_def, ei_rev,
-                                          wb, shared_sq, shared_pc);
-    k_head<<<BATCH/2, 256, 0, stream>>>(shared_sq, shared_pc, W_pt, b_pt, W_vt, b_vt,
-                                        W_vh, b_vh, tpol_h, tpol_l, val);
+    k_prep<<<384, 256, 0, stream>>>(W_adj, W_occ, W_att, W_def, W_rev, W_out, W_ph,
+                                    W_in_sq, W_in_pc, W_pt, W_vt, wb);
+    k_main<<<3072, 1024, K_SMEM, stream>>>(x_sq, x_pc, b_in_sq, b_in_pc, b_out,
+                                           ei_adj, ei_occ, ei_att, ei_def, ei_rev,
+                                           wb, shared_sq, shared_pc);
+    k_head<<<64, 512, 0, stream>>>(shared_sq, shared_pc, wb, b_pt, b_vt, W_vh, b_vh,
+                                   tpol_h, tpol_l, val);
     k_pol<<<dim3(ADIM/64, BATCH/64), 256, 0, stream>>>(tpol_h, tpol_l, wb, b_ph, pol);
 }
```

Result: slower. 211.2 us (+6.5%).
